# Kernel tuning notes

Hardware: AMD Instinct MI355X
Metric: run time of the kernel (lower is better)

Reference implementation:

```python
import jax, jax.numpy as jnp
import numpy as np
import math

S, B, E, H = 2048, 2, 1024, 16
D = E // H
LN_EPS = 1e-5


def setup_inputs() -> dict:
    key = jax.random.key(0)
    ks = jax.random.split(key, 8)
    src = jax.random.normal(ks[0], (S, B, E), dtype=jnp.float32)
    # causal attention mask: 1 = attend, 0 = masked
    src_mask = jnp.tril(jnp.ones((S, S), dtype=jnp.int32))
    in_proj_w = jax.random.normal(ks[1], (2 * E, E), dtype=jnp.float32) * 0.02
    in_proj_b = jnp.zeros((2 * E,), dtype=jnp.float32)
    out_proj_w = jax.random.normal(ks[2], (E, E), dtype=jnp.float32) * 0.02
    out_proj_b = jnp.zeros((E,), dtype=jnp.float32)
    ln_g = jnp.ones((E,), dtype=jnp.float32)
    ln_b = jnp.zeros((E,), dtype=jnp.float32)
    return {"src": src, "src_mask": src_mask, "in_proj_w": in_proj_w,
            "in_proj_b": in_proj_b, "out_proj_w": out_proj_w,
            "out_proj_b": out_proj_b, "ln_g": ln_g, "ln_b": ln_b}


def _layernorm(x, g, b):
    mu = jnp.mean(x, axis=-1, keepdims=True)
    var = jnp.mean(jnp.square(x - mu), axis=-1, keepdims=True)
    return (x - mu) * jax.lax.rsqrt(var + LN_EPS) * g + b


def reference(src, src_mask, in_proj_w, in_proj_b, out_proj_w, out_proj_b, ln_g, ln_b):
    # src: (S, B, E)
    x_norm = _layernorm(src, ln_g, ln_b)
    proj = jax.nn.silu(x_norm @ in_proj_w.T + in_proj_b)     # (S, B, 2E)
    qkv, u = jnp.split(proj, 2, axis=-1)                     # each (S, B, E)
    qkv = qkv.reshape(S, B, H, D)                            # q = k = v = qkv
    # scores: (B, H, S_q, S_k)
    scores = jnp.einsum('sbhd,tbhd->bhst', qkv, qkv) / math.sqrt(D)
    # torch does masked_fill(-inf) then silu; silu(-inf) -> 0 in the limit,
    # which is the intended semantics (masked positions contribute nothing).
    weights = jnp.where(src_mask[None, None, :, :] == 0, 0.0, jax.nn.silu(scores))
    # attn_dropout is identity at eval
    attn = jnp.einsum('bhst,tbhd->sbhd', weights, qkv).reshape(S, B, E)
    gated = attn * u
    out = src + (gated @ out_proj_w.T + out_proj_b)          # out_dropout = identity
    return out
```

## Files before the change

### kernel.cpp

```cpp
#include <hip/hip_runtime.h>


typedef __attribute__((ext_vector_type(8))) short  short8;
typedef __attribute__((ext_vector_type(4))) float  floatx4;
typedef __attribute__((ext_vector_type(4))) float  fvec4;
typedef __attribute__((ext_vector_type(4))) unsigned short usvec4;
typedef __attribute__((ext_vector_type(4))) int    intx4;

__device__ __forceinline__ unsigned short f2b(float f) {
  unsigned u = __builtin_bit_cast(unsigned, f);
  u += 0x7FFFu + ((u >> 16) & 1u);
  return (unsigned short)(u >> 16);
}
__device__ __forceinline__ float b2f(unsigned short h) {
  unsigned u = ((unsigned)h) << 16;
  return __builtin_bit_cast(float, u);
}
__device__ __forceinline__ float silu_f(float x) {
  float e = __builtin_amdgcn_exp2f(-1.44269504f * x);
  return x * __builtin_amdgcn_rcpf(1.f + e);
}
__device__ __forceinline__ void async_copy16(void* lds, const void* g) {
  __builtin_amdgcn_global_load_lds(
      (__attribute__((address_space(1))) void*)(g),
      (__attribute__((address_space(3))) void*)(lds), 16, 0, 0);
}

__global__ __launch_bounds__(256) void prep_kernel(
    const float* __restrict__ w1, unsigned short* __restrict__ w1b,
    const float* __restrict__ w2, unsigned short* __restrict__ w2b,
    const float* __restrict__ x, const float* __restrict__ g,
    const float* __restrict__ b, unsigned short* __restrict__ xn) {
  const int blk = blockIdx.x;
  if (blk < 3072) {
    int i = blk * 256 + threadIdx.x;
    const float* s; unsigned short* d; int j;
    if (i < 524288) { s = w1; d = w1b; j = i; } else { s = w2; d = w2b; j = i - 524288; }
    fvec4 v = ((const fvec4*)s)[j];
    usvec4 o = { f2b(v.x), f2b(v.y), f2b(v.z), f2b(v.w) };
    ((usvec4*)d)[j] = o;
    return;
  }
  const int lane = threadIdx.x & 63;
  const int row = (blk - 3072) * 4 + (threadIdx.x >> 6);
  const fvec4* xr = (const fvec4*)(x + (long)row * 1024);
  fvec4 v[4];
  float s = 0.f, s2 = 0.f;
  #pragma unroll
  for (int c = 0; c < 4; ++c) {
    v[c] = xr[lane + 64 * c];
    s  += v[c].x + v[c].y + v[c].z + v[c].w;
    s2 += v[c].x*v[c].x + v[c].y*v[c].y + v[c].z*v[c].z + v[c].w*v[c].w;
  }
  #pragma unroll
  for (int off = 32; off; off >>= 1) { s += __shfl_xor(s, off); s2 += __shfl_xor(s2, off); }
  float mu  = s * (1.f / 1024.f);
  float var = s2 * (1.f / 1024.f) - mu * mu;
  float rs  = rsqrtf(var + 1e-5f);
  usvec4* outr = (usvec4*)(xn + (long)row * 1024);
  #pragma unroll
  for (int c = 0; c < 4; ++c) {
    fvec4 gg = ((const fvec4*)g)[lane + 64 * c];
    fvec4 bb = ((const fvec4*)b)[lane + 64 * c];
    usvec4 o = { f2b((v[c].x - mu) * rs * gg.x + bb.x),
                 f2b((v[c].y - mu) * rs * gg.y + bb.y),
                 f2b((v[c].z - mu) * rs * gg.z + bb.z),
                 f2b((v[c].w - mu) * rs * gg.w + bb.w) };
    outr[lane + 64 * c] = o;
  }
}

__global__ __launch_bounds__(256, 2) void gemm_in(
    const unsigned short* __restrict__ A, const unsigned short* __restrict__ Bw,
    const float* __restrict__ bias,
    unsigned short* __restrict__ out0, unsigned short* __restrict__ out1) {
  __shared__ __align__(16) unsigned short sA[2][128 * 32];
  __shared__ __align__(16) unsigned short sB[2][128 * 32];
  const int t = threadIdx.x;
  const int lane = t & 63, l15 = lane & 15, quad = lane >> 4;
  const int w = t >> 6, wm = w >> 1, wn = w & 1;
  const int m0 = blockIdx.y * 128, n0 = blockIdx.x * 128;
  const int K = 1024;

  floatx4 acc[4][4];
  const floatx4 z4 = {0.f, 0.f, 0.f, 0.f};
  #pragma unroll
  for (int i = 0; i < 4; i++)
    #pragma unroll
    for (int j = 0; j < 4; j++) acc[i][j] = z4;

  for (int kt = 0; kt < 16; ++kt) {
    const int k0 = kt << 6;
    __syncthreads();
    #pragma unroll
    for (int h = 0; h < 2; ++h) {
      #pragma unroll
      for (int c = 0; c < 2; ++c) {
        int slot = c * 256 + t;
        int row = slot >> 2, col = (slot & 3) << 3;
        async_copy16(&sA[h][slot * 8], &A[(m0 + row) * K + k0 + h * 32 + col]);
        async_copy16(&sB[h][slot * 8], &Bw[(n0 + row) * K + k0 + h * 32 + col]);
      }
    }
    __syncthreads();
    #pragma unroll
    for (int h = 0; h < 2; ++h) {
      short8 af[4], bf[4];
      #pragma unroll
      for (int mr = 0; mr < 4; mr++)
        af[mr] = *(const short8*)&sA[h][(wm * 64 + mr * 16 + l15) * 32 + quad * 8];
      #pragma unroll
      for (int nr = 0; nr < 4; nr++)
        bf[nr] = *(const short8*)&sB[h][(wn * 64 + nr * 16 + l15) * 32 + quad * 8];
      #pragma unroll
      for (int mr = 0; mr < 4; mr++)
        #pragma unroll
        for (int nr = 0; nr < 4; nr++)
          acc[mr][nr] = __builtin_amdgcn_mfma_f32_16x16x32_bf16(af[mr], bf[nr], acc[mr][nr], 0, 0, 0);
    }
  }

  #pragma unroll
  for (int mr = 0; mr < 4; mr++) {
    int gm0 = m0 + wm * 64 + mr * 16 + quad * 4;
    #pragma unroll
    for (int nr = 0; nr < 4; nr++) {
      int gn = n0 + wn * 64 + nr * 16 + l15;
      float bv = bias[gn];
      unsigned short* dst = (gn < 1024) ? (out0 + gn) : (out1 + gn - 1024);
      #pragma unroll
      for (int r = 0; r < 4; r++) {
        float v = acc[mr][nr][r] + bv;
        dst[(long)(gm0 + r) * 1024] = f2b(silu_f(v));
      }
    }
  }
}

__global__ __launch_bounds__(256, 2) void gemm_out(
    const unsigned short* __restrict__ A, const unsigned short* __restrict__ Bw,
    const float* __restrict__ bias, const float* __restrict__ src,
    float* __restrict__ outf) {
  __shared__ __align__(16) unsigned short sA[2][128 * 32];
  __shared__ __align__(16) unsigned short sB[2][64 * 32];
  const int t = threadIdx.x;
  const int lane = t & 63, l15 = lane & 15, quad = lane >> 4;
  const int w = t >> 6;
  const int m0 = blockIdx.y * 128, n0 = blockIdx.x * 64;

  floatx4 acc[2][4];
  const floatx4 z4 = {0.f, 0.f, 0.f, 0.f};
  #pragma unroll
  for (int i = 0; i < 2; i++)
    #pragma unroll
    for (int j = 0; j < 4; j++) acc[i][j] = z4;

  for (int kt = 0; kt < 16; ++kt) {
    const int k0 = kt << 6;
    __syncthreads();
    #pragma unroll
    for (int h = 0; h < 2; ++h) {
      #pragma unroll
      for (int c = 0; c < 2; ++c) {
        int slot = c * 256 + t;
        int row = slot >> 2, col = (slot & 3) << 3;
        async_copy16(&sA[h][slot * 8], &A[(m0 + row) * 1024 + k0 + h * 32 + col]);
      }
      { int row = t >> 2, col = (t & 3) << 3;
        async_copy16(&sB[h][t * 8], &Bw[(n0 + row) * 1024 + k0 + h * 32 + col]); }
    }
    __syncthreads();
    #pragma unroll
    for (int h = 0; h < 2; ++h) {
      short8 af[2], bf[4];
      #pragma unroll
      for (int mr = 0; mr < 2; mr++)
        af[mr] = *(const short8*)&sA[h][(w * 32 + mr * 16 + l15) * 32 + quad * 8];
      #pragma unroll
      for (int nr = 0; nr < 4; nr++)
        bf[nr] = *(const short8*)&sB[h][(nr * 16 + l15) * 32 + quad * 8];
      #pragma unroll
      for (int mr = 0; mr < 2; mr++)
        #pragma unroll
        for (int nr = 0; nr < 4; nr++)
          acc[mr][nr] = __builtin_amdgcn_mfma_f32_16x16x32_bf16(af[mr], bf[nr], acc[mr][nr], 0, 0, 0);
    }
  }

  #pragma unroll
  for (int mr = 0; mr < 2; mr++) {
    int gm0 = m0 + w * 32 + mr * 16 + quad * 4;
    #pragma unroll
    for (int nr = 0; nr < 4; nr++) {
      int gn = n0 + nr * 16 + l15;
      float bv = bias[gn];
      #pragma unroll
      for (int r = 0; r < 4; r++) {
        long idx = (long)(gm0 + r) * 1024 + gn;
        outf[idx] = acc[mr][nr][r] + bv + src[idx];
      }
    }
  }
}

#define SKS 72
#define SVS 136
__device__ __forceinline__ void write_kv(unsigned short* sKp, unsigned short* sVp,
                                         const short8* kv, int rg, int dg, int swz0) {
  #pragma unroll
  for (int i = 0; i < 4; ++i)
    *(short8*)&sKp[(rg * 4 + i) * SKS + dg * 8] = kv[i];
  intx4 k0 = __builtin_bit_cast(intx4, kv[0]);
  intx4 k1 = __builtin_bit_cast(intx4, kv[1]);
  intx4 k2 = __builtin_bit_cast(intx4, kv[2]);
  intx4 k3 = __builtin_bit_cast(intx4, kv[3]);
  #pragma unroll
  for (int jj = 0; jj < 4; ++jj) {
    unsigned lo = __builtin_amdgcn_perm((unsigned)k1[jj], (unsigned)k0[jj], 0x05040100u);
    unsigned hi = __builtin_amdgcn_perm((unsigned)k3[jj], (unsigned)k2[jj], 0x05040100u);
    int j = 2 * jj, d = dg * 8 + j;
    int gsw = (swz0 + j) & 15;
    *(unsigned long long*)&sVp[d * SVS + gsw * 8 + (rg & 1) * 4] =
        (unsigned long long)lo | ((unsigned long long)hi << 32);
    lo = __builtin_amdgcn_perm((unsigned)k1[jj], (unsigned)k0[jj], 0x07060302u);
    hi = __builtin_amdgcn_perm((unsigned)k3[jj], (unsigned)k2[jj], 0x07060302u);
    j = 2 * jj + 1; d = dg * 8 + j;
    gsw = (swz0 + j) & 15;
    *(unsigned long long*)&sVp[d * SVS + gsw * 8 + (rg & 1) * 4] =
        (unsigned long long)lo | ((unsigned long long)hi << 32);
  }
}

template <int MODE>
__global__ __launch_bounds__(256, 2) void attn_kernel(
    const unsigned short* __restrict__ qkv, const unsigned short* __restrict__ u,
    unsigned short* __restrict__ gated) {
  __shared__ __align__(16) unsigned char smem[18432 + 2 * 17408];
  unsigned short* sK   = (unsigned short*)smem;
  unsigned short* sVt0 = (unsigned short*)(smem + 18432);
  unsigned short* sVt1 = (unsigned short*)(smem + 18432 + 17408);
  unsigned short* sQ   = sVt1;
  float*          sR   = (float*)smem;

  const int t = threadIdx.x, lane = t & 63, l15 = lane & 15, quad = lane >> 4;
  const int w = t >> 6;
  const int bh = blockIdx.x & 31;
  const int idx = (blockIdx.x >> 5) & 7, hlf = blockIdx.x >> 8;
  const int qi = (MODE == 0) ? (hlf ? (15 - idx) : idx)
                             : (hlf ? (31 - idx) : (16 + idx));
  const int b = bh >> 4, h = bh & 15;
  const long base = (long)b * 1024 + h * 64;
  const int q0 = qi * 64;
  const int nkt = (qi >> 1) + 1;
  const int rg = t >> 3, dg = t & 7;
  const int swz0 = (rg >> 1) + dg;
  const int addr_lo = 4 * (l15 + 32 * (quad & 1));
  const int addr_hi = addr_lo + 64;
  const bool qhi = quad >= 2;
  const int vswz = w * 4 + quad + (l15 & 7) + (l15 >> 3);
  const floatx4 z4 = {0.f, 0.f, 0.f, 0.f};

  #pragma unroll
  for (int c = 0; c < 2; ++c) {
    int slot = c * 256 + t, row = slot >> 3, cg = slot & 7;
    *(short8*)&sQ[row * SKS + cg * 8] =
        *(const short8*)&qkv[base + (long)(q0 + row) * 2048 + cg * 8];
  }
  __syncthreads();
  short8 qf[4][2];
  #pragma unroll
  for (int nt = 0; nt < 4; nt++)
    #pragma unroll
    for (int ks = 0; ks < 2; ks++)
      qf[nt][ks] = *(const short8*)&sQ[(nt * 16 + l15) * SKS + ks * 32 + quad * 8];
  short8 kv[4];
  #pragma unroll
  for (int i = 0; i < 4; ++i)
    kv[i] = *(const short8*)&qkv[base + (long)(rg * 4 + i) * 2048 + dg * 8];
  write_kv(sK, sVt0, kv, rg, dg, swz0);

  floatx4 oacc[4][4];
  #pragma unroll
  for (int i = 0; i < 4; i++)
    #pragma unroll
    for (int j = 0; j < 4; j++) oacc[i][j] = z4;

  for (int kt = 0; kt < nkt; ++kt) {
    unsigned short* sVtC = (kt & 1) ? sVt1 : sVt0;
    unsigned short* sVtN = (kt & 1) ? sVt0 : sVt1;
    __syncthreads();
    const bool more = (kt + 1 < nkt);
    if (more) {
      const long nb = base + (long)((kt + 1) * 128) * 2048;
      #pragma unroll
      for (int i = 0; i < 4; ++i)
        kv[i] = *(const short8*)&qkv[nb + (long)(rg * 4 + i) * 2048 + dg * 8];
    }
    short8 kf[2][2];
    #pragma unroll
    for (int mt = 0; mt < 2; mt++)
      #pragma unroll
      for (int ks = 0; ks < 2; ks++)
        kf[mt][ks] = *(const short8*)&sK[(w * 32 + mt * 16 + l15) * SKS + ks * 32 + quad * 8];
    __syncthreads();
    floatx4 sacc[2][4];
    #pragma unroll
    for (int i = 0; i < 2; i++)
      #pragma unroll
      for (int j = 0; j < 4; j++) sacc[i][j] = z4;
    #pragma unroll
    for (int ks = 0; ks < 2; ++ks)
      #pragma unroll
      for (int mt = 0; mt < 2; mt++)
        #pragma unroll
        for (int nt = 0; nt < 4; nt++)
          sacc[mt][nt] = __builtin_amdgcn_mfma_f32_16x16x32_bf16(
              kf[mt][ks], qf[nt][ks], sacc[mt][nt], 0, 0, 0);
    const bool diag = (kt == nkt - 1);
    const int tw = kt * 128 + w * 32;
    unsigned p0[2][4], p1[2][4];
    #pragma unroll
    for (int mt = 0; mt < 2; mt++)
      #pragma unroll
      for (int nt = 0; nt < 4; nt++) {
        float v[4];
        if (diag) {
          int qq = q0 + nt * 16 + l15;
          #pragma unroll
          for (int r = 0; r < 4; r++) {
            int tt = tw + mt * 16 + quad * 4 + r;
            float x = silu_f(sacc[mt][nt][r] * 0.125f);
            v[r] = (qq < tt) ? 0.f : x;
          }
        } else {
          #pragma unroll
          for (int r = 0; r < 4; r++) v[r] = silu_f(sacc[mt][nt][r] * 0.125f);
        }
        p0[mt][nt] = __builtin_amdgcn_perm(__builtin_bit_cast(unsigned, v[1]),
                                           __builtin_bit_cast(unsigned, v[0]), 0x07060302u);
        p1[mt][nt] = __builtin_amdgcn_perm(__builtin_bit_cast(unsigned, v[3]),
                                           __builtin_bit_cast(unsigned, v[2]), 0x07060302u);
      }
    short8 vb[4];
    #pragma unroll
    for (int dt = 0; dt < 4; dt++)
      vb[dt] = *(const short8*)&sVtC[(dt * 16 + l15) * SVS + ((vswz + 2 * dt) & 15) * 8];
    #pragma unroll
    for (int qt = 0; qt < 4; qt++) {
      intx4 pa;
      #pragma unroll
      for (int jj = 0; jj < 4; jj++) {
        int addr = (jj >> 1) ? addr_hi : addr_lo;
        int lo, hi;
        if (jj & 1) {
          lo = __builtin_amdgcn_ds_bpermute(addr, (int)p1[0][qt]);
          hi = __builtin_amdgcn_ds_bpermute(addr, (int)p1[1][qt]);
        } else {
          lo = __builtin_amdgcn_ds_bpermute(addr, (int)p0[0][qt]);
          hi = __builtin_amdgcn_ds_bpermute(addr, (int)p0[1][qt]);
        }
        pa[jj] = qhi ? hi : lo;
      }
      short8 paf = __builtin_bit_cast(short8, pa);
      #pragma unroll
      for (int dt = 0; dt < 4; dt++)
        oacc[qt][dt] = __builtin_amdgcn_mfma_f32_16x16x32_bf16(paf, vb[dt], oacc[qt][dt], 0, 0, 0);
    }
    if (more) write_kv(sK, sVtN, kv, rg, dg, swz0);
  }

  __syncthreads();
  float* plane = sR + (w & 1) * 4352;
  if (w < 2) {
    #pragma unroll
    for (int qt = 0; qt < 4; qt++)
      #pragma unroll
      for (int dt = 0; dt < 4; dt++)
        #pragma unroll
        for (int r = 0; r < 4; r++)
          plane[(qt * 16 + quad * 4 + r) * 68 + dt * 16 + l15] = oacc[qt][dt][r];
  }
  __syncthreads();
  if (w >= 2) {
    #pragma unroll
    for (int qt = 0; qt < 4; qt++)
      #pragma unroll
      for (int dt = 0; dt < 4; dt++)
        #pragma unroll
        for (int r = 0; r < 4; r++)
          plane[(qt * 16 + quad * 4 + r) * 68 + dt * 16 + l15] += oacc[qt][dt][r];
  }
  __syncthreads();
  {
    const int erow = t >> 2, edg = t & 3;
    const long grow = (long)(q0 + erow) * 2048 + base + edg * 16;
    short8 u0 = *(const short8*)&u[grow];
    short8 u1 = *(const short8*)&u[grow + 8];
    const float* r0p = sR + erow * 68 + edg * 16;
    const float* r1p = r0p + 4352;
    float o[16];
    #pragma unroll
    for (int c = 0; c < 4; c++) {
      fvec4 a = ((const fvec4*)r0p)[c];
      fvec4 bsum = ((const fvec4*)r1p)[c];
      o[4*c+0] = a.x + bsum.x; o[4*c+1] = a.y + bsum.y;
      o[4*c+2] = a.z + bsum.z; o[4*c+3] = a.w + bsum.w;
    }
    short8 g0, g1;
    #pragma unroll
    for (int j = 0; j < 8; ++j) {
      g0[j] = (short)f2b(o[j]     * b2f((unsigned short)u0[j]));
      g1[j] = (short)f2b(o[j + 8] * b2f((unsigned short)u1[j]));
    }
    *(short8*)&gated[grow]     = g0;
    *(short8*)&gated[grow + 8] = g1;
  }
}

extern "C" void kernel_launch(void* const* d_in, const int* in_sizes, int n_in,
                              void* d_out, int out_size, void* d_ws, size_t ws_size,
                              hipStream_t stream) {
  const float* src = (const float*)d_in[0];
  const float* w1  = (const float*)d_in[2];
  const float* b1  = (const float*)d_in[3];
  const float* w2  = (const float*)d_in[4];
  const float* b2  = (const float*)d_in[5];
  const float* lng = (const float*)d_in[6];
  const float* lnb = (const float*)d_in[7];
  float* out = (float*)d_out;

  char* ws = (char*)d_ws;
  unsigned short* xn    = (unsigned short*)(ws + 0);
  unsigned short* qkv   = (unsigned short*)(ws + 8388608);
  unsigned short* uu    = (unsigned short*)(ws + 16777216);
  unsigned short* gated = (unsigned short*)(ws + 25165824);
  unsigned short* w1b   = (unsigned short*)(ws + 33554432);
  unsigned short* w2b   = (unsigned short*)(ws + 37748736);

  prep_kernel<<<4096, 256, 0, stream>>>(w1, w1b, w2, w2b, src, lng, lnb, xn);
  gemm_in<<<dim3(16, 32), 256, 0, stream>>>(xn, w1b, b1, qkv, uu);
  attn_kernel<0><<<512, 256, 0, stream>>>(qkv, uu, gated);
  attn_kernel<1><<<512, 256, 0, stream>>>(qkv, uu, gated);
  gemm_out<<<dim3(16, 32), 256, 0, stream>>>(gated, w2b, b2, src, out);
}
```

Measured before the change: 190.8 us.

## Merge attention launches into one with 32-row query tiles and paired causal work

The two attention launches become one 1024-block launch. Each block handles a 32-row query tile from a short causal row and from its mirrored long row, so work per block is balanced. K/V double buffering is dropped to a single buffer, which cuts LDS and allows the launch bound to rise to 4 blocks per CU. In exchange, each K/V tile is now loaded by twice as many blocks, and loads no longer overlap with compute because of the single buffer and extra barriers.

```diff
diff --git a/kernel.cpp b/kernel.cpp
--- a/kernel.cpp
+++ b/kernel.cpp
@@ -231,27 +231,20 @@
   }
 }
 
-template <int MODE>
-__global__ __launch_bounds__(256, 2) void attn_kernel(
+__global__ __launch_bounds__(256, 4) void attn_kernel(
     const unsigned short* __restrict__ qkv, const unsigned short* __restrict__ u,
     unsigned short* __restrict__ gated) {
-  __shared__ __align__(16) unsigned char smem[18432 + 2 * 17408];
-  unsigned short* sK   = (unsigned short*)smem;
-  unsigned short* sVt0 = (unsigned short*)(smem + 18432);
-  unsigned short* sVt1 = (unsigned short*)(smem + 18432 + 17408);
-  unsigned short* sQ   = sVt1;
-  float*          sR   = (float*)smem;
+  __shared__ __align__(16) unsigned char smem[18432 + 17408];
+  unsigned short* sK  = (unsigned short*)smem;
+  unsigned short* sVt = (unsigned short*)(smem + 18432);
+  unsigned short* sQ  = sVt;
+  float*          sR  = (float*)smem;
 
   const int t = threadIdx.x, lane = t & 63, l15 = lane & 15, quad = lane >> 4;
   const int w = t >> 6;
-  const int bh = blockIdx.x & 31;
-  const int idx = (blockIdx.x >> 5) & 7, hlf = blockIdx.x >> 8;
-  const int qi = (MODE == 0) ? (hlf ? (15 - idx) : idx)
-                             : (hlf ? (31 - idx) : (16 + idx));
+  const int pair = blockIdx.x >> 6, sub = (blockIdx.x >> 5) & 1, bh = blockIdx.x & 31;
   const int b = bh >> 4, h = bh & 15;
   const long base = (long)b * 1024 + h * 64;
-  const int q0 = qi * 64;
-  const int nkt = (qi >> 1) + 1;
   const int rg = t >> 3, dg = t & 7;
   const int swz0 = (rg >> 1) + dg;
   const int addr_lo = 4 * (l15 + 32 * (quad & 1));
@@ -260,160 +253,149 @@
   const int vswz = w * 4 + quad + (l15 & 7) + (l15 >> 3);
   const floatx4 z4 = {0.f, 0.f, 0.f, 0.f};
 
-  #pragma unroll
-  for (int c = 0; c < 2; ++c) {
-    int slot = c * 256 + t, row = slot >> 3, cg = slot & 7;
-    *(short8*)&sQ[row * SKS + cg * 8] =
-        *(const short8*)&qkv[base + (long)(q0 + row) * 2048 + cg * 8];
-  }
-  __syncthreads();
-  short8 qf[4][2];
-  #pragma unroll
-  for (int nt = 0; nt < 4; nt++)
-    #pragma unroll
-    for (int ks = 0; ks < 2; ks++)
-      qf[nt][ks] = *(const short8*)&sQ[(nt * 16 + l15) * SKS + ks * 32 + quad * 8];
-  short8 kv[4];
-  #pragma unroll
-  for (int i = 0; i < 4; ++i)
-    kv[i] = *(const short8*)&qkv[base + (long)(rg * 4 + i) * 2048 + dg * 8];
-  write_kv(sK, sVt0, kv, rg, dg, swz0);
-
-  floatx4 oacc[4][4];
-  #pragma unroll
-  for (int i = 0; i < 4; i++)
-    #pragma unroll
-    for (int j = 0; j < 4; j++) oacc[i][j] = z4;
-
-  for (int kt = 0; kt < nkt; ++kt) {
-    unsigned short* sVtC = (kt & 1) ? sVt1 : sVt0;
-    unsigned short* sVtN = (kt & 1) ? sVt0 : sVt1;
-    __syncthreads();
-    const bool more = (kt + 1 < nkt);
-    if (more) {
-      const long nb = base + (long)((kt + 1) * 128) * 2048;
-      #pragma unroll
-      for (int i = 0; i < 4; ++i)
-        kv[i] = *(const short8*)&qkv[nb + (long)(rg * 4 + i) * 2048 + dg * 8];
-    }
-    short8 kf[2][2];
-    #pragma unroll
-    for (int mt = 0; mt < 2; mt++)
+  for (int half = 0; half < 2; ++half) {
+    const int qi = half ? (31 - pair) : pair;
+    const int q0 = qi * 64 + sub * 32;
+    const int nkt = (qi >> 1) + 1;
+
+    {
+      int row = t >> 3, cg = t & 7;
+      *(short8*)&sQ[row * SKS + cg * 8] =
+          *(const short8*)&qkv[base + (long)(q0 + row) * 2048 + cg * 8];
+    }
+    __syncthreads();
+    short8 qf[2][2];
+    #pragma unroll
+    for (int nt = 0; nt < 2; nt++)
       #pragma unroll
       for (int ks = 0; ks < 2; ks++)
-        kf[mt][ks] = *(const short8*)&sK[(w * 32 + mt * 16 + l15) * SKS + ks * 32 + quad * 8];
-    __syncthreads();
-    floatx4 sacc[2][4];
+        qf[nt][ks] = *(const short8*)&sQ[(nt * 16 + l15) * SKS + ks * 32 + quad * 8];
+    __syncthreads();
+    short8 kv[4];
+    #pragma unroll
+    for (int i = 0; i < 4; ++i)
+      kv[i] = *(const short8*)&qkv[base + (long)(rg * 4 + i) * 2048 + dg * 8];
+    write_kv(sK, sVt, kv, rg, dg, swz0);
+
+    floatx4 oacc[2][4];
     #pragma unroll
     for (int i = 0; i < 2; i++)
       #pragma unroll
-      for (int j = 0; j < 4; j++) sacc[i][j] = z4;
-    #pragma unroll
-    for (int ks = 0; ks < 2; ++ks)
+      for (int j = 0; j < 4; j++) oacc[i][j] = z4;
+
+    for (int kt = 0; kt < nkt; ++kt) {
+      __syncthreads();
+      short8 kf[2][2];
       #pragma unroll
       for (int mt = 0; mt < 2; mt++)
         #pragma unroll
-        for (int nt = 0; nt < 4; nt++)
-          sacc[mt][nt] = __builtin_amdgcn_mfma_f32_16x16x32_bf16(
-              kf[mt][ks], qf[nt][ks], sacc[mt][nt], 0, 0, 0);
-    const bool diag = (kt == nkt - 1);
-    const int tw = kt * 128 + w * 32;
-    unsigned p0[2][4], p1[2][4];
-    #pragma unroll
-    for (int mt = 0; mt < 2; mt++)
-      #pragma unroll
-      for (int nt = 0; nt < 4; nt++) {
-        float v[4];
-        if (diag) {
-          int qq = q0 + nt * 16 + l15;
+        for (int ks = 0; ks < 2; ks++)
+          kf[mt][ks] = *(const short8*)&sK[(w * 32 + mt * 16 + l15) * SKS + ks * 32 + quad * 8];
+      short8 vb[4];
+      #pragma unroll
+      for (int dt = 0; dt < 4; dt++)
+        vb[dt] = *(const short8*)&sVt[(dt * 16 + l15) * SVS + ((vswz + 2 * dt) & 15) * 8];
+      const bool more = (kt + 1 < nkt);
+      if (more) {
+        const long nb = base + (long)((kt + 1) * 128) * 2048;
+        #pragma unroll
+        for (int i = 0; i < 4; ++i)
+          kv[i] = *(const short8*)&qkv[nb + (long)(rg * 4 + i) * 2048 + dg * 8];
+      }
+      __syncthreads();
+      floatx4 sacc[2][2];
+      #pragma unroll
+      for (int i = 0; i < 2; i++) { sacc[i][0] = z4; sacc[i][1] = z4; }
+      #pragma unroll
+      for (int ks = 0; ks < 2; ++ks)
+        #pragma unroll
+        for (int mt = 0; mt < 2; mt++)
           #pragma unroll
-          for (int r = 0; r < 4; r++) {
-            int tt = tw + mt * 16 + quad * 4 + r;
-            float x = silu_f(sacc[mt][nt][r] * 0.125f);
-            v[r] = (qq < tt) ? 0.f : x;
+          for (int nt = 0; nt < 2; nt++)
+            sacc[mt][nt] = __builtin_amdgcn_mfma_f32_16x16x32_bf16(
+                kf[mt][ks], qf[nt][ks], sacc[mt][nt], 0, 0, 0);
+      const bool diag = (kt == nkt - 1);
+      const int tw = kt * 128 + w * 32;
+      unsigned p0[2][2], p1[2][2];
+      #pragma unroll
+      for (int mt = 0; mt < 2; mt++)
+        #pragma unroll
+        for (int nt = 0; nt < 2; nt++) {
+          float v[4];
+          if (diag) {
+            int qq = q0 + nt * 16 + l15;
+            #pragma unroll
+            for (int r = 0; r < 4; r++) {
+              int tt = tw + mt * 16 + quad * 4 + r;
+              float x = silu_f(sacc[mt][nt][r] * 0.125f);
+              v[r] = (qq < tt) ? 0.f : x;
+            }
+          } else {
+            #pragma unroll
+            for (int r = 0; r < 4; r++) v[r] = silu_f(sacc[mt][nt][r] * 0.125f);
           }
-        } else {
+          p0[mt][nt] = __builtin_amdgcn_perm(__builtin_bit_cast(unsigned, v[1]),
+                                             __builtin_bit_cast(unsigned, v[0]), 0x07060302u);
+          p1[mt][nt] = __builtin_amdgcn_perm(__builtin_bit_cast(unsigned, v[3]),
+                                             __builtin_bit_cast(unsigned, v[2]), 0x07060302u);
+        }
+      #pragma unroll
+      for (int qt = 0; qt < 2; qt++) {
+        intx4 pa;
+        #pragma unroll
+        for (int jj = 0; jj < 4; jj++) {
+          int addr = (jj >> 1) ? addr_hi : addr_lo;
+          int lo, hi;
+          if (jj & 1) {
+            lo = __builtin_amdgcn_ds_bpermute(addr, (int)p1[0][qt]);
+            hi = __builtin_amdgcn_ds_bpermute(addr, (int)p1[1][qt]);
+          } else {
+            lo = __builtin_amdgcn_ds_bpermute(addr, (int)p0[0][qt]);
+            hi = __builtin_amdgcn_ds_bpermute(addr, (int)p0[1][qt]);
+          }
+          pa[jj] = qhi ? hi : lo;
+        }
+        short8 paf = __builtin_bit_cast(short8, pa);
+        #pragma unroll
+        for (int dt = 0; dt < 4; dt++)
+          oacc[qt][dt] = __builtin_amdgcn_mfma_f32_16x16x32_bf16(paf, vb[dt], oacc[qt][dt], 0, 0, 0);
+      }
+      if (more) write_kv(sK, sVt, kv, rg, dg, swz0);
+    }
+
+    float* plane = sR + (w & 1) * 2176;
+    if (w < 2) {
+      #pragma unroll
+      for (int qt = 0; qt < 2; qt++)
+        #pragma unroll
+        for (int dt = 0; dt < 4; dt++)
           #pragma unroll
-          for (int r = 0; r < 4; r++) v[r] = silu_f(sacc[mt][nt][r] * 0.125f);
-        }
-        p0[mt][nt] = __builtin_amdgcn_perm(__builtin_bit_cast(unsigned, v[1]),
-                                           __builtin_bit_cast(unsigned, v[0]), 0x07060302u);
-        p1[mt][nt] = __builtin_amdgcn_perm(__builtin_bit_cast(unsigned, v[3]),
-                                           __builtin_bit_cast(unsigned, v[2]), 0x07060302u);
-      }
-    short8 vb[4];
-    #pragma unroll
-    for (int dt = 0; dt < 4; dt++)
-      vb[dt] = *(const short8*)&sVtC[(dt * 16 + l15) * SVS + ((vswz + 2 * dt) & 15) * 8];
-    #pragma unroll
-    for (int qt = 0; qt < 4; qt++) {
-      intx4 pa;
-      #pragma unroll
-      for (int jj = 0; jj < 4; jj++) {
-        int addr = (jj >> 1) ? addr_hi : addr_lo;
-        int lo, hi;
-        if (jj & 1) {
-          lo = __builtin_amdgcn_ds_bpermute(addr, (int)p1[0][qt]);
-          hi = __builtin_amdgcn_ds_bpermute(addr, (int)p1[1][qt]);
-        } else {
-          lo = __builtin_amdgcn_ds_bpermute(addr, (int)p0[0][qt]);
-          hi = __builtin_amdgcn_ds_bpermute(addr, (int)p0[1][qt]);
-        }
-        pa[jj] = qhi ? hi : lo;
-      }
-      short8 paf = __builtin_bit_cast(short8, pa);
-      #pragma unroll
-      for (int dt = 0; dt < 4; dt++)
-        oacc[qt][dt] = __builtin_amdgcn_mfma_f32_16x16x32_bf16(paf, vb[dt], oacc[qt][dt], 0, 0, 0);
-    }
-    if (more) write_kv(sK, sVtN, kv, rg, dg, swz0);
-  }
-
-  __syncthreads();
-  float* plane = sR + (w & 1) * 4352;
-  if (w < 2) {
-    #pragma unroll
-    for (int qt = 0; qt < 4; qt++)
-      #pragma unroll
-      for (int dt = 0; dt < 4; dt++)
-        #pragma unroll
-        for (int r = 0; r < 4; r++)
-          plane[(qt * 16 + quad * 4 + r) * 68 + dt * 16 + l15] = oacc[qt][dt][r];
-  }
-  __syncthreads();
-  if (w >= 2) {
-    #pragma unroll
-    for (int qt = 0; qt < 4; qt++)
-      #pragma unroll
-      for (int dt = 0; dt < 4; dt++)
-        #pragma unroll
-        for (int r = 0; r < 4; r++)
-          plane[(qt * 16 + quad * 4 + r) * 68 + dt * 16 + l15] += oacc[qt][dt][r];
-  }
-  __syncthreads();
-  {
-    const int erow = t >> 2, edg = t & 3;
-    const long grow = (long)(q0 + erow) * 2048 + base + edg * 16;
-    short8 u0 = *(const short8*)&u[grow];
-    short8 u1 = *(const short8*)&u[grow + 8];
-    const float* r0p = sR + erow * 68 + edg * 16;
-    const float* r1p = r0p + 4352;
-    float o[16];
-    #pragma unroll
-    for (int c = 0; c < 4; c++) {
-      fvec4 a = ((const fvec4*)r0p)[c];
-      fvec4 bsum = ((const fvec4*)r1p)[c];
-      o[4*c+0] = a.x + bsum.x; o[4*c+1] = a.y + bsum.y;
-      o[4*c+2] = a.z + bsum.z; o[4*c+3] = a.w + bsum.w;
-    }
-    short8 g0, g1;
-    #pragma unroll
-    for (int j = 0; j < 8; ++j) {
-      g0[j] = (short)f2b(o[j]     * b2f((unsigned short)u0[j]));
-      g1[j] = (short)f2b(o[j + 8] * b2f((unsigned short)u1[j]));
-    }
-    *(short8*)&gated[grow]     = g0;
-    *(short8*)&gated[grow + 8] = g1;
+          for (int r = 0; r < 4; r++)
+            plane[(qt * 16 + quad * 4 + r) * 68 + dt * 16 + l15] = oacc[qt][dt][r];
+    }
+    __syncthreads();
+    if (w >= 2) {
+      #pragma unroll
+      for (int qt = 0; qt < 2; qt++)
+        #pragma unroll
+        for (int dt = 0; dt < 4; dt++)
+          #pragma unroll
+          for (int r = 0; r < 4; r++)
+            plane[(qt * 16 + quad * 4 + r) * 68 + dt * 16 + l15] += oacc[qt][dt][r];
+    }
+    __syncthreads();
+    {
+      const int erow = t >> 3, edg = t & 7;
+      const long grow = (long)(q0 + erow) * 2048 + base + edg * 8;
+      short8 u0 = *(const short8*)&u[grow];
+      const float* r0p = sR + erow * 68 + edg * 8;
+      const float* r1p = r0p + 2176;
+      short8 g0;
+      #pragma unroll
+      for (int j = 0; j < 8; ++j)
+        g0[j] = (short)f2b((r0p[j] + r1p[j]) * b2f((unsigned short)u0[j]));
+      *(short8*)&gated[grow] = g0;
+    }
   }
 }
 
@@ -439,7 +421,6 @@
 
   prep_kernel<<<4096, 256, 0, stream>>>(w1, w1b, w2, w2b, src, lng, lnb, xn);
   gemm_in<<<dim3(16, 32), 256, 0, stream>>>(xn, w1b, b1, qkv, uu);
-  attn_kernel<0><<<512, 256, 0, stream>>>(qkv, uu, gated);
-  attn_kernel<1><<<512, 256, 0, stream>>>(qkv, uu, gated);
+  attn_kernel<<<1024, 256, 0, stream>>>(qkv, uu, gated);
   gemm_out<<<dim3(16, 32), 256, 0, stream>>>(gated, w2b, b2, src, out);
 }
```

Result: slower. 199.0 us (+4.3%).

## Double-buffer GEMM shared tiles and merge attention passes into one balanced launch

Applied to the files above, without the earlier changes.

Both GEMM kernels now keep two shared-memory tile buffers. Each iteration issues the async copies for the next K-tile before running the MFMAs on the current one, so global loads overlap with compute and one barrier per iteration goes away. The two templated attention launches become a single launch where each block handles query tile qi and then tile 31-qi, which evens out causal work per block and removes a kernel launch. The cost is doubled GEMM LDS use, which may affect occupancy, and a longer serial loop per attention block.

```diff
diff --git a/kernel.cpp b/kernel.cpp
--- a/kernel.cpp
+++ b/kernel.cpp
@@ -74,8 +74,8 @@
     const unsigned short* __restrict__ A, const unsigned short* __restrict__ Bw,
     const float* __restrict__ bias,
     unsigned short* __restrict__ out0, unsigned short* __restrict__ out1) {
-  __shared__ __align__(16) unsigned short sA[2][128 * 32];
-  __shared__ __align__(16) unsigned short sB[2][128 * 32];
+  __shared__ __align__(16) unsigned short sA[2][2][128 * 32];
+  __shared__ __align__(16) unsigned short sB[2][2][128 * 32];
   const int t = threadIdx.x;
   const int lane = t & 63, l15 = lane & 15, quad = lane >> 4;
   const int w = t >> 6, wm = w >> 1, wn = w & 1;
@@ -89,29 +89,38 @@
     #pragma unroll
     for (int j = 0; j < 4; j++) acc[i][j] = z4;
 
+  #pragma unroll
+  for (int h = 0; h < 2; ++h)
+    #pragma unroll
+    for (int c = 0; c < 2; ++c) {
+      int slot = c * 256 + t, row = slot >> 2, col = (slot & 3) << 3;
+      async_copy16(&sA[0][h][slot * 8], &A[(m0 + row) * K + h * 32 + col]);
+      async_copy16(&sB[0][h][slot * 8], &Bw[(n0 + row) * K + h * 32 + col]);
+    }
+
   for (int kt = 0; kt < 16; ++kt) {
-    const int k0 = kt << 6;
-    __syncthreads();
-    #pragma unroll
-    for (int h = 0; h < 2; ++h) {
-      #pragma unroll
-      for (int c = 0; c < 2; ++c) {
-        int slot = c * 256 + t;
-        int row = slot >> 2, col = (slot & 3) << 3;
-        async_copy16(&sA[h][slot * 8], &A[(m0 + row) * K + k0 + h * 32 + col]);
-        async_copy16(&sB[h][slot * 8], &Bw[(n0 + row) * K + k0 + h * 32 + col]);
-      }
-    }
-    __syncthreads();
+    const int buf = kt & 1;
+    __syncthreads();
+    if (kt + 1 < 16) {
+      const int k0 = (kt + 1) << 6;
+      #pragma unroll
+      for (int h = 0; h < 2; ++h)
+        #pragma unroll
+        for (int c = 0; c < 2; ++c) {
+          int slot = c * 256 + t, row = slot >> 2, col = (slot & 3) << 3;
+          async_copy16(&sA[buf ^ 1][h][slot * 8], &A[(m0 + row) * K + k0 + h * 32 + col]);
+          async_copy16(&sB[buf ^ 1][h][slot * 8], &Bw[(n0 + row) * K + k0 + h * 32 + col]);
+        }
+    }
     #pragma unroll
     for (int h = 0; h < 2; ++h) {
       short8 af[4], bf[4];
       #pragma unroll
       for (int mr = 0; mr < 4; mr++)
-        af[mr] = *(const short8*)&sA[h][(wm * 64 + mr * 16 + l15) * 32 + quad * 8];
+        af[mr] = *(const short8*)&sA[buf][h][(wm * 64 + mr * 16 + l15) * 32 + quad * 8];
       #pragma unroll
       for (int nr = 0; nr < 4; nr++)
-        bf[nr] = *(const short8*)&sB[h][(wn * 64 + nr * 16 + l15) * 32 + quad * 8];
+        bf[nr] = *(const short8*)&sB[buf][h][(wn * 64 + nr * 16 + l15) * 32 + quad * 8];
       #pragma unroll
       for (int mr = 0; mr < 4; mr++)
         #pragma unroll
@@ -141,8 +150,8 @@
     const unsigned short* __restrict__ A, const unsigned short* __restrict__ Bw,
     const float* __restrict__ bias, const float* __restrict__ src,
     float* __restrict__ outf) {
-  __shared__ __align__(16) unsigned short sA[2][128 * 32];
-  __shared__ __align__(16) unsigned short sB[2][64 * 32];
+  __shared__ __align__(16) unsigned short sA[2][2][128 * 32];
+  __shared__ __align__(16) unsigned short sB[2][2][64 * 32];
   const int t = threadIdx.x;
   const int lane = t & 63, l15 = lane & 15, quad = lane >> 4;
   const int w = t >> 6;
@@ -155,30 +164,42 @@
     #pragma unroll
     for (int j = 0; j < 4; j++) acc[i][j] = z4;
 
+  #pragma unroll
+  for (int h = 0; h < 2; ++h) {
+    #pragma unroll
+    for (int c = 0; c < 2; ++c) {
+      int slot = c * 256 + t, row = slot >> 2, col = (slot & 3) << 3;
+      async_copy16(&sA[0][h][slot * 8], &A[(m0 + row) * 1024 + h * 32 + col]);
+    }
+    { int row = t >> 2, col = (t & 3) << 3;
+      async_copy16(&sB[0][h][t * 8], &Bw[(n0 + row) * 1024 + h * 32 + col]); }
+  }
+
   for (int kt = 0; kt < 16; ++kt) {
-    const int k0 = kt << 6;
-    __syncthreads();
-    #pragma unroll
-    for (int h = 0; h < 2; ++h) {
-      #pragma unroll
-      for (int c = 0; c < 2; ++c) {
-        int slot = c * 256 + t;
-        int row = slot >> 2, col = (slot & 3) << 3;
-        async_copy16(&sA[h][slot * 8], &A[(m0 + row) * 1024 + k0 + h * 32 + col]);
-      }
-      { int row = t >> 2, col = (t & 3) << 3;
-        async_copy16(&sB[h][t * 8], &Bw[(n0 + row) * 1024 + k0 + h * 32 + col]); }
-    }
-    __syncthreads();
+    const int buf = kt & 1;
+    __syncthreads();
+    if (kt + 1 < 16) {
+      const int k0 = (kt + 1) << 6;
+      #pragma unroll
+      for (int h = 0; h < 2; ++h) {
+        #pragma unroll
+        for (int c = 0; c < 2; ++c) {
+          int slot = c * 256 + t, row = slot >> 2, col = (slot & 3) << 3;
+          async_copy16(&sA[buf ^ 1][h][slot * 8], &A[(m0 + row) * 1024 + k0 + h * 32 + col]);
+        }
+        { int row = t >> 2, col = (t & 3) << 3;
+          async_copy16(&sB[buf ^ 1][h][t * 8], &Bw[(n0 + row) * 1024 + k0 + h * 32 + col]); }
+      }
+    }
     #pragma unroll
     for (int h = 0; h < 2; ++h) {
       short8 af[2], bf[4];
       #pragma unroll
       for (int mr = 0; mr < 2; mr++)
-        af[mr] = *(const short8*)&sA[h][(w * 32 + mr * 16 + l15) * 32 + quad * 8];
+        af[mr] = *(const short8*)&sA[buf][h][(w * 32 + mr * 16 + l15) * 32 + quad * 8];
       #pragma unroll
       for (int nr = 0; nr < 4; nr++)
-        bf[nr] = *(const short8*)&sB[h][(nr * 16 + l15) * 32 + quad * 8];
+        bf[nr] = *(const short8*)&sB[buf][h][(nr * 16 + l15) * 32 + quad * 8];
       #pragma unroll
       for (int mr = 0; mr < 2; mr++)
         #pragma unroll
@@ -231,7 +252,6 @@
   }
 }
 
-template <int MODE>
 __global__ __launch_bounds__(256, 2) void attn_kernel(
     const unsigned short* __restrict__ qkv, const unsigned short* __restrict__ u,
     unsigned short* __restrict__ gated) {
@@ -244,14 +264,9 @@
 
   const int t = threadIdx.x, lane = t & 63, l15 = lane & 15, quad = lane >> 4;
   const int w = t >> 6;
-  const int bh = blockIdx.x & 31;
-  const int idx = (blockIdx.x >> 5) & 7, hlf = blockIdx.x >> 8;
-  const int qi = (MODE == 0) ? (hlf ? (15 - idx) : idx)
-                             : (hlf ? (31 - idx) : (16 + idx));
+  const int pair = blockIdx.x >> 5, bh = blockIdx.x & 31;
   const int b = bh >> 4, h = bh & 15;
   const long base = (long)b * 1024 + h * 64;
-  const int q0 = qi * 64;
-  const int nkt = (qi >> 1) + 1;
   const int rg = t >> 3, dg = t & 7;
   const int swz0 = (rg >> 1) + dg;
   const int addr_lo = 4 * (l15 + 32 * (quad & 1));
@@ -260,160 +275,167 @@
   const int vswz = w * 4 + quad + (l15 & 7) + (l15 >> 3);
   const floatx4 z4 = {0.f, 0.f, 0.f, 0.f};
 
-  #pragma unroll
-  for (int c = 0; c < 2; ++c) {
-    int slot = c * 256 + t, row = slot >> 3, cg = slot & 7;
-    *(short8*)&sQ[row * SKS + cg * 8] =
-        *(const short8*)&qkv[base + (long)(q0 + row) * 2048 + cg * 8];
-  }
-  __syncthreads();
-  short8 qf[4][2];
-  #pragma unroll
-  for (int nt = 0; nt < 4; nt++)
-    #pragma unroll
-    for (int ks = 0; ks < 2; ks++)
-      qf[nt][ks] = *(const short8*)&sQ[(nt * 16 + l15) * SKS + ks * 32 + quad * 8];
-  short8 kv[4];
-  #pragma unroll
-  for (int i = 0; i < 4; ++i)
-    kv[i] = *(const short8*)&qkv[base + (long)(rg * 4 + i) * 2048 + dg * 8];
-  write_kv(sK, sVt0, kv, rg, dg, swz0);
-
-  floatx4 oacc[4][4];
-  #pragma unroll
-  for (int i = 0; i < 4; i++)
-    #pragma unroll
-    for (int j = 0; j < 4; j++) oacc[i][j] = z4;
-
-  for (int kt = 0; kt < nkt; ++kt) {
-    unsigned short* sVtC = (kt & 1) ? sVt1 : sVt0;
-    unsigned short* sVtN = (kt & 1) ? sVt0 : sVt1;
-    __syncthreads();
-    const bool more = (kt + 1 < nkt);
-    if (more) {
-      const long nb = base + (long)((kt + 1) * 128) * 2048;
-      #pragma unroll
-      for (int i = 0; i < 4; ++i)
-        kv[i] = *(const short8*)&qkv[nb + (long)(rg * 4 + i) * 2048 + dg * 8];
-    }
-    short8 kf[2][2];
-    #pragma unroll
-    for (int mt = 0; mt < 2; mt++)
+  for (int half = 0; half < 2; ++half) {
+    const int qi = half ? (31 - pair) : pair;
+    const int q0 = qi * 64;
+    const int nkt = (qi >> 1) + 1;
+
+    if (half) __syncthreads();
+    #pragma unroll
+    for (int c = 0; c < 2; ++c) {
+      int slot = c * 256 + t, row = slot >> 3, cg = slot & 7;
+      *(short8*)&sQ[row * SKS + cg * 8] =
+          *(const short8*)&qkv[base + (long)(q0 + row) * 2048 + cg * 8];
+    }
+    __syncthreads();
+    short8 qf[4][2];
+    #pragma unroll
+    for (int nt = 0; nt < 4; nt++)
       #pragma unroll
       for (int ks = 0; ks < 2; ks++)
-        kf[mt][ks] = *(const short8*)&sK[(w * 32 + mt * 16 + l15) * SKS + ks * 32 + quad * 8];
-    __syncthreads();
-    floatx4 sacc[2][4];
-    #pragma unroll
-    for (int i = 0; i < 2; i++)
-      #pragma unroll
-      for (int j = 0; j < 4; j++) sacc[i][j] = z4;
-    #pragma unroll
-    for (int ks = 0; ks < 2; ++ks)
+        qf[nt][ks] = *(const short8*)&sQ[(nt * 16 + l15) * SKS + ks * 32 + quad * 8];
+    short8 kv[4];
+    #pragma unroll
+    for (int i = 0; i < 4; ++i)
+      kv[i] = *(const short8*)&qkv[base + (long)(rg * 4 + i) * 2048 + dg * 8];
+    write_kv(sK, sVt0, kv, rg, dg, swz0);
+
+    floatx4 oacc[4][4];
+    #pragma unroll
+    for (int i = 0; i < 4; i++)
+      #pragma unroll
+      for (int j = 0; j < 4; j++) oacc[i][j] = z4;
+
+    for (int kt = 0; kt < nkt; ++kt) {
+      unsigned short* sVtC = (kt & 1) ? sVt1 : sVt0;
+      unsigned short* sVtN = (kt & 1) ? sVt0 : sVt1;
+      __syncthreads();
+      const bool more = (kt + 1 < nkt);
+      if (more) {
+        const long nb = base + (long)((kt + 1) * 128) * 2048;
+        #pragma unroll
+        for (int i = 0; i < 4; ++i)
+          kv[i] = *(const short8*)&qkv[nb + (long)(rg * 4 + i) * 2048 + dg * 8];
+      }
+      short8 kf[2][2];
       #pragma unroll
       for (int mt = 0; mt < 2; mt++)
         #pragma unroll
-        for (int nt = 0; nt < 4; nt++)
-          sacc[mt][nt] = __builtin_amdgcn_mfma_f32_16x16x32_bf16(
-              kf[mt][ks], qf[nt][ks], sacc[mt][nt], 0, 0, 0);
-    const bool diag = (kt == nkt - 1);
-    const int tw = kt * 128 + w * 32;
-    unsigned p0[2][4], p1[2][4];
-    #pragma unroll
-    for (int mt = 0; mt < 2; mt++)
-      #pragma unroll
-      for (int nt = 0; nt < 4; nt++) {
-        float v[4];
-        if (diag) {
-          int qq = q0 + nt * 16 + l15;
+        for (int ks = 0; ks < 2; ks++)
+          kf[mt][ks] = *(const short8*)&sK[(w * 32 + mt * 16 + l15) * SKS + ks * 32 + quad * 8];
+      __syncthreads();
+      floatx4 sacc[2][4];
+      #pragma unroll
+      for (int i = 0; i < 2; i++)
+        #pragma unroll
+        for (int j = 0; j < 4; j++) sacc[i][j] = z4;
+      #pragma unroll
+      for (int ks = 0; ks < 2; ++ks)
+        #pragma unroll
+        for (int mt = 0; mt < 2; mt++)
           #pragma unroll
-          for (int r = 0; r < 4; r++) {
-            int tt = tw + mt * 16 + quad * 4 + r;
-            float x = silu_f(sacc[mt][nt][r] * 0.125f);
-            v[r] = (qq < tt) ? 0.f : x;
+          for (int nt = 0; nt < 4; nt++)
+            sacc[mt][nt] = __builtin_amdgcn_mfma_f32_16x16x32_bf16(
+                kf[mt][ks], qf[nt][ks], sacc[mt][nt], 0, 0, 0);
+      const bool diag = (kt == nkt - 1);
+      const int tw = kt * 128 + w * 32;
+      unsigned p0[2][4], p1[2][4];
+      #pragma unroll
+      for (int mt = 0; mt < 2; mt++)
+        #pragma unroll
+        for (int nt = 0; nt < 4; nt++) {
+          float v[4];
+          if (diag) {
+            int qq = q0 + nt * 16 + l15;
+            #pragma unroll
+            for (int r = 0; r < 4; r++) {
+              int tt = tw + mt * 16 + quad * 4 + r;
+              float x = silu_f(sacc[mt][nt][r] * 0.125f);
+              v[r] = (qq < tt) ? 0.f : x;
+            }
+          } else {
+            #pragma unroll
+            for (int r = 0; r < 4; r++) v[r] = silu_f(sacc[mt][nt][r] * 0.125f);
           }
-        } else {
+          p0[mt][nt] = __builtin_amdgcn_perm(__builtin_bit_cast(unsigned, v[1]),
+                                             __builtin_bit_cast(unsigned, v[0]), 0x07060302u);
+          p1[mt][nt] = __builtin_amdgcn_perm(__builtin_bit_cast(unsigned, v[3]),
+                                             __builtin_bit_cast(unsigned, v[2]), 0x07060302u);
+        }
+      short8 vb[4];
+      #pragma unroll
+      for (int dt = 0; dt < 4; dt++)
+        vb[dt] = *(const short8*)&sVtC[(dt * 16 + l15) * SVS + ((vswz + 2 * dt) & 15) * 8];
+      #pragma unroll
+      for (int qt = 0; qt < 4; qt++) {
+        intx4 pa;
+        #pragma unroll
+        for (int jj = 0; jj < 4; jj++) {
+          int addr = (jj >> 1) ? addr_hi : addr_lo;
+          int lo, hi;
+          if (jj & 1) {
+            lo = __builtin_amdgcn_ds_bpermute(addr, (int)p1[0][qt]);
+            hi = __builtin_amdgcn_ds_bpermute(addr, (int)p1[1][qt]);
+          } else {
+            lo = __builtin_amdgcn_ds_bpermute(addr, (int)p0[0][qt]);
+            hi = __builtin_amdgcn_ds_bpermute(addr, (int)p0[1][qt]);
+          }
+          pa[jj] = qhi ? hi : lo;
+        }
+        short8 paf = __builtin_bit_cast(short8, pa);
+        #pragma unroll
+        for (int dt = 0; dt < 4; dt++)
+          oacc[qt][dt] = __builtin_amdgcn_mfma_f32_16x16x32_bf16(paf, vb[dt], oacc[qt][dt], 0, 0, 0);
+      }
+      if (more) write_kv(sK, sVtN, kv, rg, dg, swz0);
+    }
+
+    __syncthreads();
+    float* plane = sR + (w & 1) * 4352;
+    if (w < 2) {
+      #pragma unroll
+      for (int qt = 0; qt < 4; qt++)
+        #pragma unroll
+        for (int dt = 0; dt < 4; dt++)
           #pragma unroll
-          for (int r = 0; r < 4; r++) v[r] = silu_f(sacc[mt][nt][r] * 0.125f);
-        }
-        p0[mt][nt] = __builtin_amdgcn_perm(__builtin_bit_cast(unsigned, v[1]),
-                                           __builtin_bit_cast(unsigned, v[0]), 0x07060302u);
-        p1[mt][nt] = __builtin_amdgcn_perm(__builtin_bit_cast(unsigned, v[3]),
-                                           __builtin_bit_cast(unsigned, v[2]), 0x07060302u);
-      }
-    short8 vb[4];
-    #pragma unroll
-    for (int dt = 0; dt < 4; dt++)
-      vb[dt] = *(const short8*)&sVtC[(dt * 16 + l15) * SVS + ((vswz + 2 * dt) & 15) * 8];
-    #pragma unroll
-    for (int qt = 0; qt < 4; qt++) {
-      intx4 pa;
-      #pragma unroll
-      for (int jj = 0; jj < 4; jj++) {
-        int addr = (jj >> 1) ? addr_hi : addr_lo;
-        int lo, hi;
-        if (jj & 1) {
-          lo = __builtin_amdgcn_ds_bpermute(addr, (int)p1[0][qt]);
-          hi = __builtin_amdgcn_ds_bpermute(addr, (int)p1[1][qt]);
-        } else {
-          lo = __builtin_amdgcn_ds_bpermute(addr, (int)p0[0][qt]);
-          hi = __builtin_amdgcn_ds_bpermute(addr, (int)p0[1][qt]);
-        }
-        pa[jj] = qhi ? hi : lo;
-      }
-      short8 paf = __builtin_bit_cast(short8, pa);
-      #pragma unroll
-      for (int dt = 0; dt < 4; dt++)
-        oacc[qt][dt] = __builtin_amdgcn_mfma_f32_16x16x32_bf16(paf, vb[dt], oacc[qt][dt], 0, 0, 0);
-    }
-    if (more) write_kv(sK, sVtN, kv, rg, dg, swz0);
-  }
-
-  __syncthreads();
-  float* plane = sR + (w & 1) * 4352;
-  if (w < 2) {
-    #pragma unroll
-    for (int qt = 0; qt < 4; qt++)
-      #pragma unroll
-      for (int dt = 0; dt < 4; dt++)
-        #pragma unroll
-        for (int r = 0; r < 4; r++)
-          plane[(qt * 16 + quad * 4 + r) * 68 + dt * 16 + l15] = oacc[qt][dt][r];
-  }
-  __syncthreads();
-  if (w >= 2) {
-    #pragma unroll
-    for (int qt = 0; qt < 4; qt++)
-      #pragma unroll
-      for (int dt = 0; dt < 4; dt++)
-        #pragma unroll
-        for (int r = 0; r < 4; r++)
-          plane[(qt * 16 + quad * 4 + r) * 68 + dt * 16 + l15] += oacc[qt][dt][r];
-  }
-  __syncthreads();
-  {
-    const int erow = t >> 2, edg = t & 3;
-    const long grow = (long)(q0 + erow) * 2048 + base + edg * 16;
-    short8 u0 = *(const short8*)&u[grow];
-    short8 u1 = *(const short8*)&u[grow + 8];
-    const float* r0p = sR + erow * 68 + edg * 16;
-    const float* r1p = r0p + 4352;
-    float o[16];
-    #pragma unroll
-    for (int c = 0; c < 4; c++) {
-      fvec4 a = ((const fvec4*)r0p)[c];
-      fvec4 bsum = ((const fvec4*)r1p)[c];
-      o[4*c+0] = a.x + bsum.x; o[4*c+1] = a.y + bsum.y;
-      o[4*c+2] = a.z + bsum.z; o[4*c+3] = a.w + bsum.w;
-    }
-    short8 g0, g1;
-    #pragma unroll
-    for (int j = 0; j < 8; ++j) {
-      g0[j] = (short)f2b(o[j]     * b2f((unsigned short)u0[j]));
-      g1[j] = (short)f2b(o[j + 8] * b2f((unsigned short)u1[j]));
-    }
-    *(short8*)&gated[grow]     = g0;
-    *(short8*)&gated[grow + 8] = g1;
+          for (int r = 0; r < 4; r++)
+            plane[(qt * 16 + quad * 4 + r) * 68 + dt * 16 + l15] = oacc[qt][dt][r];
+    }
+    __syncthreads();
+    if (w >= 2) {
+      #pragma unroll
+      for (int qt = 0; qt < 4; qt++)
+        #pragma unroll
+        for (int dt = 0; dt < 4; dt++)
+          #pragma unroll
+          for (int r = 0; r < 4; r++)
+            plane[(qt * 16 + quad * 4 + r) * 68 + dt * 16 + l15] += oacc[qt][dt][r];
+    }
+    __syncthreads();
+    {
+      const int erow = t >> 2, edg = t & 3;
+      const long grow = (long)(q0 + erow) * 2048 + base + edg * 16;
+      short8 u0 = *(const short8*)&u[grow];
+      short8 u1 = *(const short8*)&u[grow + 8];
+      const float* r0p = sR + erow * 68 + edg * 16;
+      const float* r1p = r0p + 4352;
+      float o[16];
+      #pragma unroll
+      for (int c = 0; c < 4; c++) {
+        fvec4 a = ((const fvec4*)r0p)[c];
+        fvec4 bsum = ((const fvec4*)r1p)[c];
+        o[4*c+0] = a.x + bsum.x; o[4*c+1] = a.y + bsum.y;
+        o[4*c+2] = a.z + bsum.z; o[4*c+3] = a.w + bsum.w;
+      }
+      short8 g0, g1;
+      #pragma unroll
+      for (int j = 0; j < 8; ++j) {
+        g0[j] = (short)f2b(o[j]     * b2f((unsigned short)u0[j]));
+        g1[j] = (short)f2b(o[j + 8] * b2f((unsigned short)u1[j]));
+      }
+      *(short8*)&gated[grow]     = g0;
+      *(short8*)&gated[grow + 8] = g1;
+    }
   }
 }
 
@@ -439,7 +461,6 @@
 
   prep_kernel<<<4096, 256, 0, stream>>>(w1, w1b, w2, w2b, src, lng, lnb, xn);
   gemm_in<<<dim3(16, 32), 256, 0, stream>>>(xn, w1b, b1, qkv, uu);
-  attn_kernel<0><<<512, 256, 0, stream>>>(qkv, uu, gated);
-  attn_kernel<1><<<512, 256, 0, stream>>>(qkv, uu, gated);
+  attn_kernel<<<512, 256, 0, stream>>>(qkv, uu, gated);
   gemm_out<<<dim3(16, 32), 256, 0, stream>>>(gated, w2b, b2, src, out);
 }
```

New measurement: 192.9 us. No clear change (+1.1%).
